# Optimization experiments

Hardware: AMD Instinct MI355X
Metric: run time of the kernel (lower is better)

## Reference

```python
import jax, jax.numpy as jnp
import numpy as np

N, E = 50000, 600000
IN, H, C = 128, 8, 32
HC = H * C
LAT, OUT, NCOM = 32, 64, 30
BN_EPS = 1e-5
NEG_SLOPE = 0.2


def setup_inputs() -> dict:
    key = jax.random.key(0)
    ks = jax.random.split(key, 32)
    f32 = jnp.float32
    def rn(i, shape, s=0.05):
        return jax.random.normal(ks[i], shape, f32) * s
    inp = {
        'x': jax.random.normal(ks[0], (N, IN), f32),
        'eps': jax.random.normal(ks[1], (N, LAT), f32),
        'edge_index': jax.random.randint(ks[2], (2, E), 0, N, jnp.int32),
        # GAT layer 1 (in -> H*C)
        'gat1_W': rn(3, (IN, HC)), 'gat1_asrc': rn(4, (H, C)), 'gat1_adst': rn(5, (H, C)), 'gat1_b': jnp.zeros((HC,), f32),
        'bn1_g': jnp.ones((HC,), f32), 'bn1_b': jnp.zeros((HC,), f32),
        # GAT layer 2 (H*C -> H*C)
        'gat2_W': rn(6, (HC, HC)), 'gat2_asrc': rn(7, (H, C)), 'gat2_adst': rn(8, (H, C)), 'gat2_b': jnp.zeros((HC,), f32),
        'bn2_g': jnp.ones((HC,), f32), 'bn2_b': jnp.zeros((HC,), f32),
        # GAT layer 3 (H*C -> H*C)
        'gat3_W': rn(9, (HC, HC)), 'gat3_asrc': rn(10, (H, C)), 'gat3_adst': rn(11, (H, C)), 'gat3_b': jnp.zeros((HC,), f32),
        'bn3_g': jnp.ones((HC,), f32), 'bn3_b': jnp.zeros((HC,), f32),
        # heads
        'res_W': rn(12, (IN, HC)), 'res_b': jnp.zeros((HC,), f32),
        'mu_W': rn(13, (HC, LAT)), 'mu_b': jnp.zeros((LAT,), f32),
        'lv_W': rn(14, (HC, LAT)), 'lv_b': jnp.zeros((LAT,), f32),
        'dec_W': rn(15, (LAT, OUT)), 'dec_b': jnp.zeros((OUT,), f32),
        'aux_W': rn(16, (HC, NCOM)), 'aux_b': jnp.zeros((NCOM,), f32),
    }
    return inp


def gat_conv(x, src, dst, W, asrc, adst, b):
    # PyG GATConv (concat=True, self-loops already in src/dst, lin bias=False)
    n = x.shape[0]
    h = (x @ W).reshape(n, H, C)                      # [N,H,C]
    a_s = jnp.einsum('nhc,hc->nh', h, asrc)           # [N,H]
    a_d = jnp.einsum('nhc,hc->nh', h, adst)
    e = jax.nn.leaky_relu(a_s[src] + a_d[dst], NEG_SLOPE)  # [E,H]
    m = jax.ops.segment_max(e, dst, num_segments=n)        # per-dest softmax (stable)
    p = jnp.exp(e - m[dst])
    s = jax.ops.segment_sum(p, dst, num_segments=n)
    alpha = p / (s[dst] + 1e-16)                      # [E,H]
    out = jax.ops.segment_sum(h[src] * alpha[:, :, None], dst, num_segments=n)
    return out.reshape(n, HC) + b


def batch_norm(x, g, b):
    mu = x.mean(0)
    var = x.var(0)  # biased var, as torch BN uses for normalization
    return (x - mu) * jax.lax.rsqrt(var + BN_EPS) * g + b


def reference(x, eps, edge_index,
              gat1_W, gat1_asrc, gat1_adst, gat1_b, bn1_g, bn1_b,
              gat2_W, gat2_asrc, gat2_adst, gat2_b, bn2_g, bn2_b,
              gat3_W, gat3_asrc, gat3_adst, gat3_b, bn3_g, bn3_b,
              res_W, res_b, mu_W, mu_b, lv_W, lv_b, dec_W, dec_b, aux_W, aux_b):
    loops = jnp.arange(N, dtype=edge_index.dtype)
    src = jnp.concatenate([edge_index[0], loops])
    dst = jnp.concatenate([edge_index[1], loops])

    residual = x @ res_W + res_b
    h = jax.nn.relu(batch_norm(gat_conv(x, src, dst, gat1_W, gat1_asrc, gat1_adst, gat1_b), bn1_g, bn1_b))
    h = jax.nn.relu(batch_norm(gat_conv(h, src, dst, gat2_W, gat2_asrc, gat2_adst, gat2_b), bn2_g, bn2_b))
    h = jax.nn.relu(batch_norm(gat_conv(h, src, dst, gat3_W, gat3_asrc, gat3_adst, gat3_b), bn3_g, bn3_b))
    h = h + residual

    mu = h @ mu_W + mu_b
    logvar = h @ lv_W + lv_b
    z = mu + eps * jnp.exp(0.5 * logvar)   # reparameterize
    out = z @ dec_W + dec_b
    aux = h @ aux_W + aux_b
    return (out, mu, logvar, aux)
```

## Files before the change

kernel.cpp:

```cpp
#include <hip/hip_runtime.h>

#define N_NODES 50000
#define N_EDGES 600000
#define HC 256
#define NH 8
#define AGG_BLOCKS 2048
#define AGG_WAVES (AGG_BLOCKS * 4)

typedef short s8v __attribute__((ext_vector_type(8)));
typedef float f4v __attribute__((ext_vector_type(4)));
typedef _Float16 h4v __attribute__((ext_vector_type(4)));
typedef _Float16 h8v __attribute__((ext_vector_type(8)));
typedef __attribute__((address_space(1))) const unsigned int as1_cu32;
typedef __attribute__((address_space(3))) unsigned int as3_u32;

__device__ inline ushort f2bf(float f) {
  unsigned u = __float_as_uint(f);
  unsigned r = u + 0x7FFF + ((u >> 16) & 1);
  return (ushort)(r >> 16);
}

__global__ void k_init_cnt(int* __restrict__ cnt) {
  int i = blockIdx.x * 256 + threadIdx.x;
  if (i < N_NODES) cnt[i] = 1;
}

__global__ void k_count(const int* __restrict__ dstE, int* __restrict__ cnt) {
  int e = blockIdx.x * 256 + threadIdx.x;
  if (e < N_EDGES) atomicAdd(&cnt[dstE[e]], 1);
}

__global__ void k_scan_bsum(const int* __restrict__ cnt, int* __restrict__ bsum) {
  __shared__ int sd[256];
  int i = blockIdx.x * 256 + threadIdx.x;
  sd[threadIdx.x] = (i < N_NODES) ? cnt[i] : 0;
  __syncthreads();
  for (int o = 128; o > 0; o >>= 1) {
    if (threadIdx.x < o) sd[threadIdx.x] += sd[threadIdx.x + o];
    __syncthreads();
  }
  if (threadIdx.x == 0) bsum[blockIdx.x] = sd[0];
}

__global__ void k_scan_offsets(int* __restrict__ bsum, int nb) {
  __shared__ int s[256];
  int t = threadIdx.x;
  int v = (t < nb) ? bsum[t] : 0;
  s[t] = v; __syncthreads();
  for (int o = 1; o < 256; o <<= 1) {
    int x = (t >= o) ? s[t - o] : 0;
    __syncthreads();
    s[t] += x;
    __syncthreads();
  }
  if (t < nb) bsum[t] = s[t] - v;
}

__global__ void k_scan_write(const int* __restrict__ cnt, const int* __restrict__ bsum,
                             int* __restrict__ rowptr, int* __restrict__ fillptr) {
  __shared__ int s[256];
  int t = threadIdx.x;
  int i = blockIdx.x * 256 + t;
  int v = (i < N_NODES) ? cnt[i] : 0;
  s[t] = v; __syncthreads();
  for (int o = 1; o < 256; o <<= 1) {
    int x = (t >= o) ? s[t - o] : 0;
    __syncthreads();
    s[t] += x;
    __syncthreads();
  }
  int excl = s[t] - v + bsum[blockIdx.x];
  if (i < N_NODES) {
    rowptr[i] = excl;
    fillptr[i] = excl;
    if (i == N_NODES - 1) rowptr[N_NODES] = excl + v;
  }
}

__global__ void k_fill(const int* __restrict__ srcE, const int* __restrict__ dstE,
                       int* __restrict__ fillptr, int* __restrict__ srcs) {
  int i = blockIdx.x * 256 + threadIdx.x;
  if (i < N_NODES) {
    int pos = atomicAdd(&fillptr[i], 1);
    srcs[pos] = i;
  } else if (i < N_NODES + N_EDGES) {
    int e = i - N_NODES;
    int pos = atomicAdd(&fillptr[dstE[e]], 1);
    srcs[pos] = srcE[e];
  }
}

__global__ void k_cvt_x(const float* __restrict__ X, ushort* __restrict__ Xb) {
  size_t i = ((size_t)blockIdx.x * 256 + threadIdx.x) * 4;
  float4 x4 = *(const float4*)&X[i];
  ushort4 o;
  o.x = f2bf(x4.x); o.y = f2bf(x4.y); o.z = f2bf(x4.z); o.w = f2bf(x4.w);
  *(ushort4*)&Xb[i] = o;
}

__global__ void k_cvt_wt(const float* __restrict__ W, ushort* __restrict__ Wt, int K, int Nw) {
  __shared__ ushort s[32][33];
  int tx = threadIdx.x & 31, ty = threadIdx.x >> 5;
  int k0 = blockIdx.x * 32, n0 = blockIdx.y * 32;
  for (int j = 0; j < 32; j += 8)
    s[ty + j][tx] = f2bf(W[(size_t)(k0 + ty + j) * Nw + n0 + tx]);
  __syncthreads();
  for (int j = 0; j < 32; j += 8)
    Wt[(size_t)(n0 + ty + j) * K + k0 + tx] = s[tx][ty + j];
}

__global__ void k_pack_head(const float* __restrict__ muW, const float* __restrict__ lvW,
                            const float* __restrict__ auxW, ushort* __restrict__ Wth) {
  int n = blockIdx.x;
  int k = threadIdx.x;
  float v = 0.f;
  if (n < 32) v = muW[k * 32 + n];
  else if (n < 64) v = lvW[k * 32 + (n - 32)];
  else if (n < 94) v = auxW[k * 30 + (n - 64)];
  Wth[n * 256 + k] = f2bf(v);
}

template <typename OutT>
__launch_bounds__(256)
__global__ void k_gemm_bf16(const ushort* __restrict__ A, const ushort* __restrict__ Wt,
                            const float* __restrict__ bias, int bias_off, OutT* __restrict__ Out,
                            int M, int K, int ldc) {
  __shared__ __align__(16) ushort As[16 * 512];
  __shared__ __align__(16) ushort Bs[16 * 512];
  int t = threadIdx.x, w = t >> 6, L = t & 63;
  int bm = blockIdx.x * 128, bn = blockIdx.y * 128;
  int lrow = L & 15, lcol = (L >> 4) * 8;

  const ushort* ga[4];
  const ushort* gb[4];
#pragma unroll
  for (int u = 0; u < 4; u++) {
    int i = w * 4 + u;
    int mt = i >> 1, ks = i & 1;
    int arow = bm + mt * 16 + lrow;
    if (arow >= M) arow = M - 1;
    ga[u] = A + (size_t)arow * K + ks * 32 + lcol;
    int brow = bn + mt * 16 + lrow;
    gb[u] = Wt + (size_t)brow * K + ks * 32 + lcol;
  }

  f4v acc[4][4];
  f4v zero = {0.f, 0.f, 0.f, 0.f};
#pragma unroll
  for (int mi = 0; mi < 4; mi++)
#pragma unroll
    for (int ni = 0; ni < 4; ni++) acc[mi][ni] = zero;

  int wm = (w >> 1) * 4;
  int wn = (w & 1) * 4;

  int nk = K >> 6;
  for (int kt = 0; kt < nk; kt++) {
#pragma unroll
    for (int u = 0; u < 4; u++) {
      int i = w * 4 + u;
      __builtin_amdgcn_global_load_lds((as1_cu32*)ga[u], (as3_u32*)&As[i * 512], 16, 0, 0);
      __builtin_amdgcn_global_load_lds((as1_cu32*)gb[u], (as3_u32*)&Bs[i * 512], 16, 0, 0);
      ga[u] += 64; gb[u] += 64;
    }
    __syncthreads();
#pragma unroll
    for (int ks = 0; ks < 2; ks++) {
      s8v af[4], bf[4];
#pragma unroll
      for (int mi = 0; mi < 4; mi++)
        af[mi] = *(const s8v*)&As[(((wm + mi) * 2 + ks) * 64 + L) * 8];
#pragma unroll
      for (int ni = 0; ni < 4; ni++)
        bf[ni] = *(const s8v*)&Bs[(((wn + ni) * 2 + ks) * 64 + L) * 8];
#pragma unroll
      for (int mi = 0; mi < 4; mi++)
#pragma unroll
        for (int ni = 0; ni < 4; ni++)
          acc[mi][ni] = __builtin_amdgcn_mfma_f32_16x16x32_bf16(af[mi], bf[ni], acc[mi][ni], 0, 0, 0);
    }
    __syncthreads();
  }
#pragma unroll
  for (int ni = 0; ni < 4; ni++) {
    int col = bn + (wn + ni) * 16 + (L & 15);
    float bb = (bias && col >= bias_off) ? bias[col - bias_off] : 0.f;
#pragma unroll
    for (int mi = 0; mi < 4; mi++) {
      int rbase = bm + (wm + mi) * 16 + (L >> 4) * 4;
#pragma unroll
      for (int i = 0; i < 4; i++) {
        int r = rbase + i;
        if (r < M) Out[(size_t)r * ldc + col] = (OutT)(acc[mi][ni][i] + bb);
      }
    }
  }
}

__launch_bounds__(256)
__global__ void k_att(const _Float16* __restrict__ B, int ld, const float* __restrict__ asrc,
                      const float* __restrict__ adst,
                      float* __restrict__ as_, float* __restrict__ ad_) {
  int wid = (blockIdx.x * 256 + threadIdx.x) >> 6;
  int lane = threadIdx.x & 63;
  h4v x = *(const h4v*)&B[(size_t)wid * ld + (lane << 2)];
  float4 s4 = *(const float4*)&asrc[lane << 2];
  float4 d4 = *(const float4*)&adst[lane << 2];
  float x0 = (float)x[0], x1 = (float)x[1], x2 = (float)x[2], x3 = (float)x[3];
  float vs = x0 * s4.x + x1 * s4.y + x2 * s4.z + x3 * s4.w;
  float vd = x0 * d4.x + x1 * d4.y + x2 * d4.z + x3 * d4.w;
  vs += __shfl_xor(vs, 1); vs += __shfl_xor(vs, 2); vs += __shfl_xor(vs, 4);
  vd += __shfl_xor(vd, 1); vd += __shfl_xor(vd, 2); vd += __shfl_xor(vd, 4);
  if ((lane & 7) == 0) {
    as_[wid * NH + (lane >> 3)] = vs;
    ad_[wid * NH + (lane >> 3)] = vd;
  }
}

#define FMA4(P, B2)                                                                        \
  asm("v_fma_mix_f32 %0, %1, %2, %0 op_sel:[0,0,0] op_sel_hi:[0,1,0]"                      \
      : "+v"(ac0) : "v"(P), "v"((B2).x));                                                  \
  asm("v_fma_mix_f32 %0, %1, %2, %0 op_sel:[0,1,0] op_sel_hi:[0,1,0]"                      \
      : "+v"(ac1) : "v"(P), "v"((B2).x));                                                  \
  asm("v_fma_mix_f32 %0, %1, %2, %0 op_sel:[0,0,0] op_sel_hi:[0,1,0]"                      \
      : "+v"(ac2) : "v"(P), "v"((B2).y));                                                  \
  asm("v_fma_mix_f32 %0, %1, %2, %0 op_sel:[0,1,0] op_sel_hi:[0,1,0]"                      \
      : "+v"(ac3) : "v"(P), "v"((B2).y));

__launch_bounds__(256)
__global__ void k_agg(const int* __restrict__ rowptr, const int* __restrict__ srcs,
                      const float* __restrict__ as_, const float* __restrict__ ad_,
                      const _Float16* __restrict__ B, int ld, const float* __restrict__ gb,
                      _Float16* __restrict__ C, float* __restrict__ part,
                      float* __restrict__ stats) {
  __shared__ float ss[4 * 512];
  int t = threadIdx.x;
  if (blockIdx.x == 0) {
    stats[t] = 0.f; stats[t + 256] = 0.f;
  }
  int w = t >> 6, lane = t & 63;
  int h = lane >> 3;
  int cb = lane << 2;
  int ldu = ld >> 2;
  const uint2* Bu = (const uint2*)B;
  float4 g4 = *(const float4*)&gb[cb];
  float sts0 = 0.f, sts1 = 0.f, sts2 = 0.f, sts3 = 0.f;
  float stq0 = 0.f, stq1 = 0.f, stq2 = 0.f, stq3 = 0.f;

  for (int n = blockIdx.x * 4 + w; n < N_NODES; n += AGG_WAVES) {
    int beg = rowptr[n], end = rowptr[n + 1];
    float ad_nh = ad_[n * NH + h];
    float ac0 = 0.f, ac1 = 0.f, ac2 = 0.f, ac3 = 0.f, wsum = 0.f;
    int k = beg;
    for (; k + 4 <= end; k += 4) {
      int s0 = srcs[k], s1 = srcs[k + 1], s2 = srcs[k + 2], s3 = srcs[k + 3];
      uint2 b0 = Bu[(size_t)s0 * ldu + lane];
      uint2 b1 = Bu[(size_t)s1 * ldu + lane];
      uint2 b2 = Bu[(size_t)s2 * ldu + lane];
      uint2 b3 = Bu[(size_t)s3 * ldu + lane];
      float e0 = as_[s0 * NH + h] + ad_nh; e0 = e0 > 0.f ? e0 : 0.2f * e0;
      float e1 = as_[s1 * NH + h] + ad_nh; e1 = e1 > 0.f ? e1 : 0.2f * e1;
      float e2 = as_[s2 * NH + h] + ad_nh; e2 = e2 > 0.f ? e2 : 0.2f * e2;
      float e3 = as_[s3 * NH + h] + ad_nh; e3 = e3 > 0.f ? e3 : 0.2f * e3;
      float p0 = __expf(e0), p1 = __expf(e1), p2 = __expf(e2), p3 = __expf(e3);
      wsum += (p0 + p1) + (p2 + p3);
      FMA4(p0, b0)
      FMA4(p1, b1)
      FMA4(p2, b2)
      FMA4(p3, b3)
    }
    for (; k < end; k++) {
      int s = srcs[k];
      h4v b4 = *(const h4v*)&B[(size_t)s * ld + cb];
      float e = as_[s * NH + h] + ad_nh;
      e = e > 0.f ? e : 0.2f * e;
      float p = __expf(e);
      wsum += p;
      ac0 += p * (float)b4[0]; ac1 += p * (float)b4[1];
      ac2 += p * (float)b4[2]; ac3 += p * (float)b4[3];
    }
    float inv = 1.f / (wsum + 1e-16f);
    float v0 = ac0 * inv + g4.x, v1 = ac1 * inv + g4.y;
    float v2 = ac2 * inv + g4.z, v3 = ac3 * inv + g4.w;
    h4v o; o[0] = (_Float16)v0; o[1] = (_Float16)v1; o[2] = (_Float16)v2; o[3] = (_Float16)v3;
    *(h4v*)&C[(size_t)n * 256 + cb] = o;
    sts0 += v0; stq0 += v0 * v0;
    sts1 += v1; stq1 += v1 * v1;
    sts2 += v2; stq2 += v2 * v2;
    sts3 += v3; stq3 += v3 * v3;
  }
  float* sw = &ss[w * 512];
  sw[cb + 0] = sts0; sw[cb + 1] = sts1; sw[cb + 2] = sts2; sw[cb + 3] = sts3;
  sw[256 + cb + 0] = stq0; sw[256 + cb + 1] = stq1;
  sw[256 + cb + 2] = stq2; sw[256 + cb + 3] = stq3;
  __syncthreads();
  float p0 = ss[t] + ss[512 + t] + ss[1024 + t] + ss[1536 + t];
  float p1 = ss[256 + t] + ss[768 + t] + ss[1280 + t] + ss[1792 + t];
  part[(size_t)blockIdx.x * 512 + t] = p0;
  part[(size_t)blockIdx.x * 512 + 256 + t] = p1;
}

__global__ void k_bn_reduce(const float* __restrict__ part, float* __restrict__ stats) {
  int i = threadIdx.x;
  int base = blockIdx.x * (AGG_BLOCKS / 16);
  float s0 = 0.f, s1 = 0.f;
  for (int b = 0; b < AGG_BLOCKS / 16; b++) {
    s0 += part[(size_t)(base + b) * 512 + i];
    s1 += part[(size_t)(base + b) * 512 + 256 + i];
  }
  atomicAdd(&stats[i], s0);
  atomicAdd(&stats[256 + i], s1);
}

__global__ void k_bn_relu_cvt(const _Float16* __restrict__ X, const float* __restrict__ stats,
                              const float* __restrict__ g, const float* __restrict__ b,
                              const _Float16* __restrict__ resid, int rld,
                              ushort* __restrict__ Xb) {
  size_t i = ((size_t)blockIdx.x * 256 + threadIdx.x) * 8;
  int c = (int)(i & 255);
  const float invN = 1.f / (float)N_NODES;
  h8v x8 = *(const h8v*)&X[i];
  float v[8];
#pragma unroll
  for (int q = 0; q < 2; q++) {
    float4 s4 = *(const float4*)&stats[c + q * 4];
    float4 q4 = *(const float4*)&stats[256 + c + q * 4];
    float4 g4 = *(const float4*)&g[c + q * 4];
    float4 b4 = *(const float4*)&b[c + q * 4];
    float m0 = s4.x * invN, m1 = s4.y * invN, m2 = s4.z * invN, m3 = s4.w * invN;
    v[q * 4 + 0] = ((float)x8[q * 4 + 0] - m0) * rsqrtf(q4.x * invN - m0 * m0 + 1e-5f) * g4.x + b4.x;
    v[q * 4 + 1] = ((float)x8[q * 4 + 1] - m1) * rsqrtf(q4.y * invN - m1 * m1 + 1e-5f) * g4.y + b4.y;
    v[q * 4 + 2] = ((float)x8[q * 4 + 2] - m2) * rsqrtf(q4.z * invN - m2 * m2 + 1e-5f) * g4.z + b4.z;
    v[q * 4 + 3] = ((float)x8[q * 4 + 3] - m3) * rsqrtf(q4.w * invN - m3 * m3 + 1e-5f) * g4.w + b4.w;
  }
#pragma unroll
  for (int q = 0; q < 8; q++) v[q] = v[q] > 0.f ? v[q] : 0.f;
  if (resid) {
    size_t row = i >> 8;
    h8v r8 = *(const h8v*)&resid[row * rld + c];
#pragma unroll
    for (int q = 0; q < 8; q++) v[q] += (float)r8[q];
  }
  ushort o8[8];
#pragma unroll
  for (int q = 0; q < 8; q++) o8[q] = f2bf(v[q]);
  *(uint4*)&Xb[i] = *(const uint4*)o8;
}

__launch_bounds__(256)
__global__ void k_dec(const _Float16* __restrict__ Hd, const float* __restrict__ eps,
                      const float* __restrict__ mub, const float* __restrict__ lvb,
                      const float* __restrict__ auxb,
                      const float* __restrict__ decW, const float* __restrict__ decb,
                      float* __restrict__ out) {
  __shared__ float wsd[2048];
  __shared__ float shz[4][32];
  int t = threadIdx.x;
  for (int i = t; i < 2048; i += 256) wsd[i] = decW[i];
  int w = t >> 6, lane = t & 63;
  int n = blockIdx.x * 4 + w;
  const _Float16* hd = &Hd[(size_t)n * 128];
  if (lane < 32) {
    float mu = (float)hd[lane] + mub[lane];
    float lv = (float)hd[32 + lane] + lvb[lane];
    out[(size_t)N_NODES * 64 + (size_t)n * 32 + lane] = mu;
    out[(size_t)N_NODES * 96 + (size_t)n * 32 + lane] = lv;
    shz[w][lane] = mu + eps[(size_t)n * 32 + lane] * __expf(0.5f * lv);
  } else if (lane < 62) {
    int j = lane - 32;
    out[(size_t)N_NODES * 128 + (size_t)n * 30 + j] = (float)hd[64 + j] + auxb[j];
  }
  __syncthreads();
  float o = decb[lane];
#pragma unroll 8
  for (int k = 0; k < 32; k++) o += shz[w][k] * wsd[k * 64 + lane];
  out[(size_t)n * 64 + lane] = o;
}

extern "C" void kernel_launch(void* const* d_in, const int* in_sizes, int n_in,
                              void* d_out, int out_size, void* d_ws, size_t ws_size,
                              hipStream_t stream) {
  (void)in_sizes; (void)n_in; (void)out_size; (void)ws_size;
  const float* x    = (const float*)d_in[0];
  const float* eps  = (const float*)d_in[1];
  const int*   ei   = (const int*)d_in[2];
  const float* gW[3]    = {(const float*)d_in[3],  (const float*)d_in[9],  (const float*)d_in[15]};
  const float* gasrc[3] = {(const float*)d_in[4],  (const float*)d_in[10], (const float*)d_in[16]};
  const float* gadst[3] = {(const float*)d_in[5],  (const float*)d_in[11], (const float*)d_in[17]};
  const float* gbias[3] = {(const float*)d_in[6],  (const float*)d_in[12], (const float*)d_in[18]};
  const float* bng[3]   = {(const float*)d_in[7],  (const float*)d_in[13], (const float*)d_in[19]};
  const float* bnb[3]   = {(const float*)d_in[8],  (const float*)d_in[14], (const float*)d_in[20]};
  const float* resW = (const float*)d_in[21];
  const float* resb = (const float*)d_in[22];
  const float* muW  = (const float*)d_in[23];
  const float* mub  = (const float*)d_in[24];
  const float* lvW  = (const float*)d_in[25];
  const float* lvb  = (const float*)d_in[26];
  const float* decW = (const float*)d_in[27];
  const float* decb = (const float*)d_in[28];
  const float* auxW = (const float*)d_in[29];
  const float* auxb = (const float*)d_in[30];
  float* out = (float*)d_out;

  char* ws = (char*)d_ws;
  size_t off = 0;
  auto alloc = [&](size_t bytes) -> void* {
    void* p = ws + off;
    off += (bytes + 255) & ~(size_t)255;
    return p;
  };
  _Float16* X0R = (_Float16*)alloc((size_t)N_NODES * 512 * 2);
  _Float16* X0  = (_Float16*)alloc((size_t)N_NODES * HC * 2);
  _Float16* X1  = (_Float16*)alloc((size_t)N_NODES * HC * 2);
  _Float16* Hd  = (_Float16*)alloc((size_t)N_NODES * 128 * 2);
  ushort* Xb    = (ushort*)alloc((size_t)N_NODES * HC * 2);
  float*  as_   = (float*)alloc((size_t)N_NODES * NH * 4);
  float*  ad_   = (float*)alloc((size_t)N_NODES * NH * 4);
  float*  stats = (float*)alloc(512 * 4);
  float*  part  = (float*)alloc((size_t)AGG_BLOCKS * 512 * 4);
  int* cnt      = (int*)alloc((size_t)N_NODES * 4);
  int* rowptr   = (int*)alloc((size_t)(N_NODES + 1) * 4);
  int* fillptr  = (int*)alloc((size_t)N_NODES * 4);
  int* srcs     = (int*)alloc((size_t)(N_NODES + N_EDGES) * 4);
  int* bsum     = (int*)alloc(256 * 4);
  ushort* WtP   = (ushort*)alloc(512 * 128 * 2);
  ushort* Wt2   = (ushort*)alloc(256 * 256 * 2);
  ushort* Wt3   = (ushort*)alloc(256 * 256 * 2);
  ushort* Wth   = (ushort*)alloc(128 * 256 * 2);

  const int NB = (N_NODES + 255) / 256;
  k_init_cnt<<<NB, 256, 0, stream>>>(cnt);
  k_count<<<(N_EDGES + 255) / 256, 256, 0, stream>>>(ei + N_EDGES, cnt);
  k_scan_bsum<<<NB, 256, 0, stream>>>(cnt, bsum);
  k_scan_offsets<<<1, 256, 0, stream>>>(bsum, NB);
  k_scan_write<<<NB, 256, 0, stream>>>(cnt, bsum, rowptr, fillptr);
  k_fill<<<(N_NODES + N_EDGES + 255) / 256, 256, 0, stream>>>(ei, ei + N_EDGES, fillptr, srcs);

  k_cvt_wt<<<dim3(4, 8), 256, 0, stream>>>(gW[0], WtP, 128, 256);
  k_cvt_wt<<<dim3(4, 8), 256, 0, stream>>>(resW, WtP + 256 * 128, 128, 256);
  k_cvt_wt<<<dim3(8, 8), 256, 0, stream>>>(gW[1], Wt2, 256, 256);
  k_cvt_wt<<<dim3(8, 8), 256, 0, stream>>>(gW[2], Wt3, 256, 256);
  k_pack_head<<<128, 256, 0, stream>>>(muW, lvW, auxW, Wth);
  k_cvt_x<<<(N_NODES * 128) / 1024, 256, 0, stream>>>(x, Xb);

  const int GM = (N_NODES + 127) / 128;
  const int EW_GRID = (N_NODES * HC) / 2048;

  k_gemm_bf16<_Float16><<<dim3(GM, 4), 256, 0, stream>>>(Xb, WtP, resb, 256, X0R, N_NODES, 128, 512);
  k_att<<<N_NODES / 4, 256, 0, stream>>>(X0R, 512, gasrc[0], gadst[0], as_, ad_);
  k_agg<<<AGG_BLOCKS, 256, 0, stream>>>(rowptr, srcs, as_, ad_, X0R, 512, gbias[0], X1, part, stats);
  k_bn_reduce<<<16, 256, 0, stream>>>(part, stats);
  k_bn_relu_cvt<<<EW_GRID, 256, 0, stream>>>(X1, stats, bng[0], bnb[0], nullptr, 0, Xb);

  const ushort* Wts[2] = {Wt2, Wt3};
  for (int L = 0; L < 2; L++) {
    k_gemm_bf16<_Float16><<<dim3(GM, 2), 256, 0, stream>>>(Xb, Wts[L], nullptr, 0, X0, N_NODES, 256, 256);
    k_att<<<N_NODES / 4, 256, 0, stream>>>(X0, 256, gasrc[L + 1], gadst[L + 1], as_, ad_);
    k_agg<<<AGG_BLOCKS, 256, 0, stream>>>(rowptr, srcs, as_, ad_, X0, 256, gbias[L + 1], X1, part, stats);
    k_bn_reduce<<<16, 256, 0, stream>>>(part, stats);
    k_bn_relu_cvt<<<EW_GRID, 256, 0, stream>>>(
        X1, stats, bng[L + 1], bnb[L + 1], (L == 1) ? (X0R + 256) : nullptr, 512, Xb);
  }
  k_gemm_bf16<_Float16><<<dim3(GM, 1), 256, 0, stream>>>(Xb, Wth, nullptr, 0, Hd, N_NODES, 256, 128);
  k_dec<<<N_NODES / 4, 256, 0, stream>>>(Hd, eps, mub, lvb, auxb, decW, decb, out);
}
```

Baseline: 644.9 us.

## Fuse attention logits into GEMM epilogue, fuse head GEMM with decoder, merge prep kernels

```diff
diff --git a/kernel.cpp b/kernel.cpp
--- a/kernel.cpp
+++ b/kernel.cpp
@@ -98,33 +98,57 @@
   *(ushort4*)&Xb[i] = o;
 }
 
-__global__ void k_cvt_wt(const float* __restrict__ W, ushort* __restrict__ Wt, int K, int Nw) {
+__global__ void k_prep(const float* __restrict__ gW0, const float* __restrict__ resW,
+                       const float* __restrict__ gW1, const float* __restrict__ gW2,
+                       const float* __restrict__ muW, const float* __restrict__ lvW,
+                       const float* __restrict__ auxW,
+                       ushort* __restrict__ WtP, ushort* __restrict__ Wt2,
+                       ushort* __restrict__ Wt3, ushort* __restrict__ Wth) {
   __shared__ ushort s[32][33];
-  int tx = threadIdx.x & 31, ty = threadIdx.x >> 5;
-  int k0 = blockIdx.x * 32, n0 = blockIdx.y * 32;
-  for (int j = 0; j < 32; j += 8)
-    s[ty + j][tx] = f2bf(W[(size_t)(k0 + ty + j) * Nw + n0 + tx]);
-  __syncthreads();
-  for (int j = 0; j < 32; j += 8)
-    Wt[(size_t)(n0 + ty + j) * K + k0 + tx] = s[tx][ty + j];
-}
-
-__global__ void k_pack_head(const float* __restrict__ muW, const float* __restrict__ lvW,
-                            const float* __restrict__ auxW, ushort* __restrict__ Wth) {
-  int n = blockIdx.x;
-  int k = threadIdx.x;
-  float v = 0.f;
-  if (n < 32) v = muW[k * 32 + n];
-  else if (n < 64) v = lvW[k * 32 + (n - 32)];
-  else if (n < 94) v = auxW[k * 30 + (n - 64)];
-  Wth[n * 256 + k] = f2bf(v);
+  int id = blockIdx.x;
+  int t = threadIdx.x;
+  if (id < 64) {
+    const float* W = (id < 32) ? gW0 : resW;
+    ushort* Wt = (id < 32) ? WtP : (WtP + 256 * 128);
+    int a = id & 31;
+    int bx = a & 3, by = a >> 2;
+    int tx = t & 31, ty = t >> 5;
+    int k0 = bx * 32, n0 = by * 32;
+    for (int j = 0; j < 32; j += 8)
+      s[ty + j][tx] = f2bf(W[(size_t)(k0 + ty + j) * 256 + n0 + tx]);
+    __syncthreads();
+    for (int j = 0; j < 32; j += 8)
+      Wt[(size_t)(n0 + ty + j) * 128 + k0 + tx] = s[tx][ty + j];
+  } else if (id < 192) {
+    const float* W = (id < 128) ? gW1 : gW2;
+    ushort* Wt = (id < 128) ? Wt2 : Wt3;
+    int a = (id - 64) & 63;
+    int bx = a & 7, by = a >> 3;
+    int tx = t & 31, ty = t >> 5;
+    int k0 = bx * 32, n0 = by * 32;
+    for (int j = 0; j < 32; j += 8)
+      s[ty + j][tx] = f2bf(W[(size_t)(k0 + ty + j) * 256 + n0 + tx]);
+    __syncthreads();
+    for (int j = 0; j < 32; j += 8)
+      Wt[(size_t)(n0 + ty + j) * 256 + k0 + tx] = s[tx][ty + j];
+  } else {
+    int n = id - 192;
+    int k = t;
+    float v = 0.f;
+    if (n < 32) v = muW[k * 32 + n];
+    else if (n < 64) v = lvW[k * 32 + (n - 32)];
+    else if (n < 94) v = auxW[k * 30 + (n - 64)];
+    Wth[n * 256 + k] = f2bf(v);
+  }
 }
 
 template <typename OutT>
 __launch_bounds__(256)
 __global__ void k_gemm_bf16(const ushort* __restrict__ A, const ushort* __restrict__ Wt,
                             const float* __restrict__ bias, int bias_off, OutT* __restrict__ Out,
-                            int M, int K, int ldc) {
+                            int M, int K, int ldc,
+                            const float* __restrict__ att_asrc, const float* __restrict__ att_adst,
+                            float* __restrict__ att_as, float* __restrict__ att_ad) {
   __shared__ __align__(16) ushort As[16 * 512];
   __shared__ __align__(16) ushort Bs[16 * 512];
   int t = threadIdx.x, w = t >> 6, L = t & 63;
@@ -195,25 +219,141 @@
       }
     }
   }
+  if (att_as && bn < 256) {
+    int hb = ((unsigned)(bn + wn * 16)) >> 5;
+    int cl = L & 15;
+    float sa[4], da[4];
+#pragma unroll
+    for (int ni = 0; ni < 4; ni++) {
+      int h = hb + (ni >> 1);
+      int cih = (ni & 1) * 16 + cl;
+      sa[ni] = att_asrc[h * 32 + cih];
+      da[ni] = att_adst[h * 32 + cih];
+    }
+#pragma unroll
+    for (int hi = 0; hi < 2; hi++) {
+#pragma unroll
+      for (int mi = 0; mi < 4; mi++) {
+#pragma unroll
+        for (int i = 0; i < 4; i++) {
+          float vs = acc[mi][hi * 2][i] * sa[hi * 2] + acc[mi][hi * 2 + 1][i] * sa[hi * 2 + 1];
+          float vd = acc[mi][hi * 2][i] * da[hi * 2] + acc[mi][hi * 2 + 1][i] * da[hi * 2 + 1];
+          vs += __shfl_xor(vs, 1); vd += __shfl_xor(vd, 1);
+          vs += __shfl_xor(vs, 2); vd += __shfl_xor(vd, 2);
+          vs += __shfl_xor(vs, 4); vd += __shfl_xor(vd, 4);
+          vs += __shfl_xor(vs, 8); vd += __shfl_xor(vd, 8);
+          int r = bm + (wm + mi) * 16 + (L >> 4) * 4 + i;
+          if (cl == 0 && r < M) {
+            att_as[r * NH + hb + hi] = vs;
+            att_ad[r * NH + hb + hi] = vd;
+          }
+        }
+      }
+    }
+  }
 }
 
 __launch_bounds__(256)
-__global__ void k_att(const _Float16* __restrict__ B, int ld, const float* __restrict__ asrc,
-                      const float* __restrict__ adst,
-                      float* __restrict__ as_, float* __restrict__ ad_) {
-  int wid = (blockIdx.x * 256 + threadIdx.x) >> 6;
-  int lane = threadIdx.x & 63;
-  h4v x = *(const h4v*)&B[(size_t)wid * ld + (lane << 2)];
-  float4 s4 = *(const float4*)&asrc[lane << 2];
-  float4 d4 = *(const float4*)&adst[lane << 2];
-  float x0 = (float)x[0], x1 = (float)x[1], x2 = (float)x[2], x3 = (float)x[3];
-  float vs = x0 * s4.x + x1 * s4.y + x2 * s4.z + x3 * s4.w;
-  float vd = x0 * d4.x + x1 * d4.y + x2 * d4.z + x3 * d4.w;
-  vs += __shfl_xor(vs, 1); vs += __shfl_xor(vs, 2); vs += __shfl_xor(vs, 4);
-  vd += __shfl_xor(vd, 1); vd += __shfl_xor(vd, 2); vd += __shfl_xor(vd, 4);
-  if ((lane & 7) == 0) {
-    as_[wid * NH + (lane >> 3)] = vs;
-    ad_[wid * NH + (lane >> 3)] = vd;
+__global__ void k_gemm_head(const ushort* __restrict__ A, const ushort* __restrict__ Wt,
+                            const float* __restrict__ eps,
+                            const float* __restrict__ mub, const float* __restrict__ lvb,
+                            const float* __restrict__ auxb,
+                            const float* __restrict__ decW, const float* __restrict__ decb,
+                            float* __restrict__ out) {
+  __shared__ __align__(16) ushort smem[16384];
+  __shared__ float wsd[2048];
+  __shared__ float shz[4][32];
+  ushort* As = smem;
+  ushort* Bs = smem + 8192;
+  int t = threadIdx.x, w = t >> 6, L = t & 63;
+  int bm = blockIdx.x * 128;
+  int lrow = L & 15, lcol = (L >> 4) * 8;
+  const int K = 256;
+  for (int i = t; i < 2048; i += 256) wsd[i] = decW[i];
+
+  const ushort* ga[4];
+  const ushort* gb[4];
+#pragma unroll
+  for (int u = 0; u < 4; u++) {
+    int i = w * 4 + u;
+    int mt = i >> 1, ks = i & 1;
+    int arow = bm + mt * 16 + lrow;
+    if (arow >= N_NODES) arow = N_NODES - 1;
+    ga[u] = A + (size_t)arow * K + ks * 32 + lcol;
+    int brow = mt * 16 + lrow;
+    gb[u] = Wt + (size_t)brow * K + ks * 32 + lcol;
+  }
+  f4v acc[4][4];
+  f4v zero = {0.f, 0.f, 0.f, 0.f};
+#pragma unroll
+  for (int mi = 0; mi < 4; mi++)
+#pragma unroll
+    for (int ni = 0; ni < 4; ni++) acc[mi][ni] = zero;
+  int wm = (w >> 1) * 4;
+  int wn = (w & 1) * 4;
+  for (int kt = 0; kt < 4; kt++) {
+#pragma unroll
+    for (int u = 0; u < 4; u++) {
+      int i = w * 4 + u;
+      __builtin_amdgcn_global_load_lds((as1_cu32*)ga[u], (as3_u32*)&As[i * 512], 16, 0, 0);
+      __builtin_amdgcn_global_load_lds((as1_cu32*)gb[u], (as3_u32*)&Bs[i * 512], 16, 0, 0);
+      ga[u] += 64; gb[u] += 64;
+    }
+    __syncthreads();
+#pragma unroll
+    for (int ks = 0; ks < 2; ks++) {
+      s8v af[4], bf[4];
+#pragma unroll
+      for (int mi = 0; mi < 4; mi++)
+        af[mi] = *(const s8v*)&As[(((wm + mi) * 2 + ks) * 64 + L) * 8];
+#pragma unroll
+      for (int ni = 0; ni < 4; ni++)
+        bf[ni] = *(const s8v*)&Bs[(((wn + ni) * 2 + ks) * 64 + L) * 8];
+#pragma unroll
+      for (int mi = 0; mi < 4; mi++)
+#pragma unroll
+        for (int ni = 0; ni < 4; ni++)
+          acc[mi][ni] = __builtin_amdgcn_mfma_f32_16x16x32_bf16(af[mi], bf[ni], acc[mi][ni], 0, 0, 0);
+    }
+    __syncthreads();
+  }
+  _Float16* tile = (_Float16*)smem;
+#pragma unroll
+  for (int ni = 0; ni < 4; ni++) {
+    int c = (wn + ni) * 16 + (L & 15);
+#pragma unroll
+    for (int mi = 0; mi < 4; mi++) {
+      int rbase = (wm + mi) * 16 + (L >> 4) * 4;
+#pragma unroll
+      for (int i = 0; i < 4; i++)
+        tile[(rbase + i) * 128 + c] = (_Float16)acc[mi][ni][i];
+    }
+  }
+  __syncthreads();
+  for (int rr = 0; rr < 32; rr++) {
+    int rl = w * 32 + rr;
+    int n = bm + rl;
+    bool valid = n < N_NODES;
+    if (L < 32) {
+      float mu = (float)tile[rl * 128 + L] + mub[L];
+      float lv = (float)tile[rl * 128 + 32 + L] + lvb[L];
+      float zv = 0.f;
+      if (valid) {
+        out[(size_t)N_NODES * 64 + (size_t)n * 32 + L] = mu;
+        out[(size_t)N_NODES * 96 + (size_t)n * 32 + L] = lv;
+        zv = mu + eps[(size_t)n * 32 + L] * __expf(0.5f * lv);
+      }
+      shz[w][L] = zv;
+    } else if (L < 62 && valid) {
+      int j = L - 32;
+      out[(size_t)N_NODES * 128 + (size_t)n * 30 + j] = (float)tile[rl * 128 + 64 + j] + auxb[j];
+    }
+    __syncthreads();
+    float o = decb[L];
+#pragma unroll 8
+    for (int kk = 0; kk < 32; kk++) o += shz[w][kk] * wsd[kk * 64 + L];
+    if (valid) out[(size_t)n * 64 + L] = o;
+    __syncthreads();
   }
 }
 
@@ -345,36 +485,6 @@
 #pragma unroll
   for (int q = 0; q < 8; q++) o8[q] = f2bf(v[q]);
   *(uint4*)&Xb[i] = *(const uint4*)o8;
-}
-
-__launch_bounds__(256)
-__global__ void k_dec(const _Float16* __restrict__ Hd, const float* __restrict__ eps,
-                      const float* __restrict__ mub, const float* __restrict__ lvb,
-                      const float* __restrict__ auxb,
-                      const float* __restrict__ decW, const float* __restrict__ decb,
-                      float* __restrict__ out) {
-  __shared__ float wsd[2048];
-  __shared__ float shz[4][32];
-  int t = threadIdx.x;
-  for (int i = t; i < 2048; i += 256) wsd[i] = decW[i];
-  int w = t >> 6, lane = t & 63;
-  int n = blockIdx.x * 4 + w;
-  const _Float16* hd = &Hd[(size_t)n * 128];
-  if (lane < 32) {
-    float mu = (float)hd[lane] + mub[lane];
-    float lv = (float)hd[32 + lane] + lvb[lane];
-    out[(size_t)N_NODES * 64 + (size_t)n * 32 + lane] = mu;
-    out[(size_t)N_NODES * 96 + (size_t)n * 32 + lane] = lv;
-    shz[w][lane] = mu + eps[(size_t)n * 32 + lane] * __expf(0.5f * lv);
-  } else if (lane < 62) {
-    int j = lane - 32;
-    out[(size_t)N_NODES * 128 + (size_t)n * 30 + j] = (float)hd[64 + j] + auxb[j];
-  }
-  __syncthreads();
-  float o = decb[lane];
-#pragma unroll 8
-  for (int k = 0; k < 32; k++) o += shz[w][k] * wsd[k * 64 + lane];
-  out[(size_t)n * 64 + lane] = o;
 }
 
 extern "C" void kernel_launch(void* const* d_in, const int* in_sizes, int n_in,
@@ -412,7 +522,6 @@
   _Float16* X0R = (_Float16*)alloc((size_t)N_NODES * 512 * 2);
   _Float16* X0  = (_Float16*)alloc((size_t)N_NODES * HC * 2);
   _Float16* X1  = (_Float16*)alloc((size_t)N_NODES * HC * 2);
-  _Float16* Hd  = (_Float16*)alloc((size_t)N_NODES * 128 * 2);
   ushort* Xb    = (ushort*)alloc((size_t)N_NODES * HC * 2);
   float*  as_   = (float*)alloc((size_t)N_NODES * NH * 4);
   float*  ad_   = (float*)alloc((size_t)N_NODES * NH * 4);
@@ -436,31 +545,26 @@
   k_scan_write<<<NB, 256, 0, stream>>>(cnt, bsum, rowptr, fillptr);
   k_fill<<<(N_NODES + N_EDGES + 255) / 256, 256, 0, stream>>>(ei, ei + N_EDGES, fillptr, srcs);
 
-  k_cvt_wt<<<dim3(4, 8), 256, 0, stream>>>(gW[0], WtP, 128, 256);
-  k_cvt_wt<<<dim3(4, 8), 256, 0, stream>>>(resW, WtP + 256 * 128, 128, 256);
-  k_cvt_wt<<<dim3(8, 8), 256, 0, stream>>>(gW[1], Wt2, 256, 256);
-  k_cvt_wt<<<dim3(8, 8), 256, 0, stream>>>(gW[2], Wt3, 256, 256);
-  k_pack_head<<<128, 256, 0, stream>>>(muW, lvW, auxW, Wth);
+  k_prep<<<320, 256, 0, stream>>>(gW[0], resW, gW[1], gW[2], muW, lvW, auxW, WtP, Wt2, Wt3, Wth);
   k_cvt_x<<<(N_NODES * 128) / 1024, 256, 0, stream>>>(x, Xb);
 
   const int GM = (N_NODES + 127) / 128;
   const int EW_GRID = (N_NODES * HC) / 2048;
 
-  k_gemm_bf16<_Float16><<<dim3(GM, 4), 256, 0, stream>>>(Xb, WtP, resb, 256, X0R, N_NODES, 128, 512);
-  k_att<<<N_NODES / 4, 256, 0, stream>>>(X0R, 512, gasrc[0], gadst[0], as_, ad_);
+  k_gemm_bf16<_Float16><<<dim3(GM, 4), 256, 0, stream>>>(
+      Xb, WtP, resb, 256, X0R, N_NODES, 128, 512, gasrc[0], gadst[0], as_, ad_);
   k_agg<<<AGG_BLOCKS, 256, 0, stream>>>(rowptr, srcs, as_, ad_, X0R, 512, gbias[0], X1, part, stats);
   k_bn_reduce<<<16, 256, 0, stream>>>(part, stats);
   k_bn_relu_cvt<<<EW_GRID, 256, 0, stream>>>(X1, stats, bng[0], bnb[0], nullptr, 0, Xb);
 
   const ushort* Wts[2] = {Wt2, Wt3};
   for (int L = 0; L < 2; L++) {
-    k_gemm_bf16<_Float16><<<dim3(GM, 2), 256, 0, stream>>>(Xb, Wts[L], nullptr, 0, X0, N_NODES, 256, 256);
-    k_att<<<N_NODES / 4, 256, 0, stream>>>(X0, 256, gasrc[L + 1], gadst[L + 1], as_, ad_);
+    k_gemm_bf16<_Float16><<<dim3(GM, 2), 256, 0, stream>>>(
+        Xb, Wts[L], nullptr, 0, X0, N_NODES, 256, 256, gasrc[L + 1], gadst[L + 1], as_, ad_);
     k_agg<<<AGG_BLOCKS, 256, 0, stream>>>(rowptr, srcs, as_, ad_, X0, 256, gbias[L + 1], X1, part, stats);
     k_bn_reduce<<<16, 256, 0, stream>>>(part, stats);
     k_bn_relu_cvt<<<EW_GRID, 256, 0, stream>>>(
         X1, stats, bng[L + 1], bnb[L + 1], (L == 1) ? (X0R + 256) : nullptr, 512, Xb);
   }
-  k_gemm_bf16<_Float16><<<dim3(GM, 1), 256, 0, stream>>>(Xb, Wth, nullptr, 0, Hd, N_NODES, 256, 128);
-  k_dec<<<N_NODES / 4, 256, 0, stream>>>(Hd, eps, mub, lvb, auxb, decW, decb, out);
-}
+  k_gemm_head<<<GM, 256, 0, stream>>>(Xb, Wth, eps, mub, lvb, auxb, decW, decb, out);
+}
```

Result: no change. 639.7 us (-0.8%).
